# Performance work log

Hardware: AMD Instinct MI355X
Metric: run time of the kernel (lower is better)

Reference implementation:

```python
import jax, jax.numpy as jnp
import numpy as np

NINP = 256
NHID = 256
NOUT = 256
T = 128
B = 256
DIV = 10        # ceil(dt.max()/limit) with dt=1.0, limit=0.1
YCOEFF = 1.0
ZCOEFF = 1.0


def setup_inputs() -> dict:
    key = jax.random.key(0)
    ks = jax.random.split(key, 16)
    std = 1.0 / np.sqrt(NHID)
    u = lambda k, shape: jax.random.uniform(k, shape, jnp.float32, -std, std)
    inp = {
        'input': jax.random.normal(ks[0], (T, B, NINP), jnp.float32),
        'dt': jnp.ones((T, B, 1), jnp.float32),
        'W_i': u(ks[1], (4 * NHID, NINP)),  'b_i': u(ks[2], (4 * NHID,)),
        'W_h': u(ks[3], (3 * NHID, NHID)),  'b_h': u(ks[4], (3 * NHID,)),
        'W_z': u(ks[5], (NHID, NHID)),      'b_z': u(ks[6], (NHID,)),
        'W_dt': u(ks[7], (2, 1)),           'b_dt': u(ks[8], (2,)),
        'W_c': jax.random.normal(ks[9], (NOUT, NHID), jnp.float32) * np.sqrt(2.0 / NHID),
        'b_c': u(ks[10], (NOUT,)),
        'W_s': u(ks[11], (2 * NHID, 2 * NHID)), 'b_s': u(ks[12], (2 * NHID,)),
    }
    return inp


def _forward(input, dt, W_i, b_i, W_h, b_h, W_z, b_z, W_dt, b_dt, W_c, b_c, W_s, b_s):
    noise_key = jax.random.key(1234)
    H = NHID

    def outer(carry, xs):
        y, z = carry
        inp_t, dt_t, t = xs
        delta = dt_t / DIV  # [B, 1]

        def inner(c, d):
            x, y, z = c
            ti = x @ W_i.T + b_i                       # [B, 4H]
            i_dt1, i_dt2, i_z, i_y = jnp.split(ti, 4, axis=1)
            th = y @ W_h.T + b_h                       # [B, 3H]
            h_dt1, h_dt2, h_y = jnp.split(th, 3, axis=1)
            tdt = delta @ W_dt.T + b_dt                # [B, 2]
            t_dt1, t_dt2 = tdt[:, 0:1], tdt[:, 1:2]
            ms_dt_bar = jax.nn.sigmoid(t_dt1) * jax.nn.sigmoid(i_dt1 + h_dt1)
            ms_dt = jax.nn.sigmoid(t_dt2) * jax.nn.sigmoid(i_dt2 + h_dt2)
            z = (1.0 - ms_dt) * z + ms_dt * jnp.tanh(i_y + h_y)
            y = (1.0 - ms_dt_bar) * y + ms_dt_bar * jnp.tanh(z @ W_z.T + b_z + i_z)
            x = y @ W_c.T + b_c                        # classifier output fed back
            k = jax.random.fold_in(noise_key, t * DIV + d)
            noise = jax.random.normal(k, (B, 2 * H), jnp.float32)
            s = jnp.tanh(noise @ W_s.T + b_s)
            ny, nz = s[:, :H], s[:, H:]
            y = y + YCOEFF * ny * delta
            z = z + ZCOEFF * nz * delta
            return (x, y, z), None

        (x, y, z), _ = jax.lax.scan(inner, (inp_t, y, z), jnp.arange(DIV))
        return (y, z), y

    y0 = jnp.zeros((B, H), jnp.float32)
    z0 = jnp.zeros((B, H), jnp.float32)
    (_, _), y_hidds = jax.lax.scan(outer, (y0, z0), (input, dt, jnp.arange(T)))
    out = y_hidds @ W_c.T + b_c  # [T, B, NOUT]
    return out


def reference(input, dt, W_i, b_i, W_h, b_h, W_z, b_z, W_dt, b_dt, W_c, b_c, W_s, b_s):
    return _forward(input, dt, W_i, b_i, W_h, b_h, W_z, b_z, W_dt, b_dt, W_c, b_c, W_s, b_s)
```

## Files before the change

### kernel.cpp

```cpp
#include <hip/hip_runtime.h>
#include <stdint.h>


typedef __attribute__((ext_vector_type(8))) short bf16x8_t;
typedef __attribute__((ext_vector_type(4))) float f32x4_t;
typedef __attribute__((ext_vector_type(4))) unsigned int u32x4_t;
typedef unsigned short u16;

#define R_LDS_BYTES 155904

__device__ __forceinline__ float bf2f(u16 b) {
  union { uint32_t u; float f; } v; v.u = ((uint32_t)b) << 16; return v.f;
}
__device__ __forceinline__ u16 f2bf(float f) {
  union { float f; uint32_t u; } v; v.f = f;
  uint32_t x = v.u;
  return (u16)((x + 0x7FFFu + ((x >> 16) & 1u)) >> 16);
}
__device__ __forceinline__ f32x4_t mfma16(bf16x8_t a, bf16x8_t b, f32x4_t c) {
  return __builtin_amdgcn_mfma_f32_16x16x32_bf16(a, b, c, 0, 0, 0);
}
__device__ __forceinline__ float sigm(float x) { return 1.0f / (1.0f + __expf(-x)); }
__device__ __forceinline__ float tanh_f(float x) {
  float t = __expf(-2.0f * fabsf(x));
  float r = (1.0f - t) / (1.0f + t);
  return x < 0.0f ? -r : r;
}

__device__ __forceinline__ void cstore16(void* p, u32x4_t v) {
  asm volatile("global_store_dwordx4 %0, %1, off sc0 sc1" :: "v"(p), "v"(v) : "memory");
}
__device__ __forceinline__ void pollpair(const uint32_t* p, uint32_t seq,
                                         u32x4_t* a, u32x4_t* b) {
  while (true) {
    u32x4_t x, y;
    asm volatile("global_load_dwordx4 %0, %2, off sc0 sc1\n\t"
                 "global_load_dwordx4 %1, %3, off sc0 sc1\n\t"
                 "s_waitcnt vmcnt(0)"
                 : "=&v"(x), "=&v"(y) : "v"(p), "v"(p + 4) : "memory");
    if (x.y == seq && x.w == seq && y.y == seq && y.w == seq) { *a = x; *b = y; return; }
    __builtin_amdgcn_s_sleep(1);
  }
}
__device__ __forceinline__ u32x4_t cload16v(const void* p) {
  u32x4_t r;
  asm volatile("global_load_dwordx4 %0, %1, off sc0 sc1\n\ts_waitcnt vmcnt(0)"
               : "=&v"(r) : "v"(p) : "memory");
  return r;
}

__device__ __forceinline__ int fragK(int l, int e) {
  return ((l >> 4) << 2) + (e & 3) + ((e >> 2) << 4);
}
__device__ __forceinline__ int halfSlot(int h, int m) {
  return ((h >> 5) & 3) * 512 + (((((h & 15) >> 2) << 4) | m) << 3) +
         ((h & 3) | (((h >> 4) & 1) << 2));
}

__device__ __forceinline__ void threefry(uint32_t k0, uint32_t k1, uint32_t x0, uint32_t x1,
                                         uint32_t* o0, uint32_t* o1) {
  uint32_t ks2 = k0 ^ k1 ^ 0x1BD11BDAu;
  x0 += k0; x1 += k1;
#define TFR(rot) { x0 += x1; x1 = (x1 << rot) | (x1 >> (32 - rot)); x1 ^= x0; }
  TFR(13) TFR(15) TFR(26) TFR(6)   x0 += k1;  x1 += ks2 + 1u;
  TFR(17) TFR(29) TFR(16) TFR(24)  x0 += ks2; x1 += k0 + 2u;
  TFR(13) TFR(15) TFR(26) TFR(6)   x0 += k0;  x1 += k1 + 3u;
  TFR(17) TFR(29) TFR(16) TFR(24)  x0 += k1;  x1 += ks2 + 4u;
  TFR(13) TFR(15) TFR(26) TFR(6)   x0 += ks2; x1 += k0 + 5u;
#undef TFR
  *o0 = x0; *o1 = x1;
}

__device__ __forceinline__ float bits2normal(uint32_t bits) {
  union { uint32_t u; float f; } cv; cv.u = 0x3F800000u | (bits >> 9);
  float f = cv.f - 1.0f;
  float u = fmaf(f, 2.0f, -0.99999994f);
  u = fmaxf(u, -0.99999994f);
  float w = -log1pf(-u * u);
  float p;
  if (w < 5.0f) {
    w = w - 2.5f;
    p = 2.81022636e-08f;
    p = fmaf(p, w, 3.43273939e-07f);
    p = fmaf(p, w, -3.5233877e-06f);
    p = fmaf(p, w, -4.39150654e-06f);
    p = fmaf(p, w, 0.00021858087f);
    p = fmaf(p, w, -0.00125372503f);
    p = fmaf(p, w, -0.00417768164f);
    p = fmaf(p, w, 0.246640727f);
    p = fmaf(p, w, 1.50140941f);
  } else {
    w = sqrtf(w) - 3.0f;
    p = -0.000200214257f;
    p = fmaf(p, w, 0.000100950558f);
    p = fmaf(p, w, 0.00134934322f);
    p = fmaf(p, w, -0.00367342844f);
    p = fmaf(p, w, 0.00573950773f);
    p = fmaf(p, w, -0.0076224613f);
    p = fmaf(p, w, 0.00943887047f);
    p = fmaf(p, w, 1.00167406f);
    p = fmaf(p, w, 2.83297682f);
  }
  return 1.41421354f * p * u;
}

__global__ void k_prep(const float* __restrict__ W_i, const float* __restrict__ W_c,
                       const float* __restrict__ b_i, const float* __restrict__ b_c,
                       float* __restrict__ Wic, float* __restrict__ bip) {
  __shared__ float wi[256];
  __shared__ float red[256];
  int o = blockIdx.x; int tid = threadIdx.x;
  wi[tid] = W_i[o * 256 + tid];
  __syncthreads();
  float acc = 0.f;
  for (int j = 0; j < 256; ++j) acc = fmaf(wi[j], W_c[j * 256 + tid], acc);
  Wic[(size_t)o * 256 + tid] = acc;
  red[tid] = wi[tid] * b_c[tid];
  __syncthreads();
  for (int s = 128; s > 0; s >>= 1) { if (tid < s) red[tid] += red[tid + s]; __syncthreads(); }
  if (tid == 0) bip[o] = b_i[o] + red[0];
}

__global__ void k_bias(const float* __restrict__ b_i, const float* __restrict__ bip,
                       const float* __restrict__ b_h,
                       float* __restrict__ biasD0, float* __restrict__ biasDn) {
  int c = blockIdx.x * 256 + threadIdx.x;
  float bh = (c < 512) ? b_h[c] : (c >= 768 ? b_h[c - 256] : 0.f);
  biasD0[c] = b_i[c] + bh;
  biasDn[c] = bip[c] + bh;
}

__global__ void k_packw(const float* __restrict__ srcA, int rowsA, const float* __restrict__ srcB,
                        u16* __restrict__ dst, int O, int K) {
  int t = blockIdx.x * blockDim.x + threadIdx.x;
  int KK = K >> 5;
  int total = (O >> 4) * KK * 64;
  if (t >= total) return;
  int l = t & 63; int kk = (t >> 6) % KK; int to = t / (64 * KK);
  int n = (to << 4) | (l & 15);
  int kb = (kk << 5) + ((l >> 4) << 2);
  const float* src = (n < rowsA) ? (srcA + (size_t)n * K) : (srcB + (size_t)(n - rowsA) * K);
  u16 out[8];
#pragma unroll
  for (int e = 0; e < 8; ++e) out[e] = f2bf(src[kb + (e & 3) + ((e >> 2) << 4)]);
  *reinterpret_cast<uint4*>(dst + (size_t)t * 8) = *reinterpret_cast<const uint4*>(out);
}

__global__ void k_packe2(const float* __restrict__ Wic, const float* __restrict__ Wh,
                         u16* __restrict__ dst) {
  int t = blockIdx.x * blockDim.x + threadIdx.x;
  int l = t & 63; int kk = (t >> 6) & 7; int to = t >> 9;
  int n = (to << 4) | (l & 15);
  int kb = (kk << 5) + ((l >> 4) << 2);
  u16 out[8];
#pragma unroll
  for (int e = 0; e < 8; ++e) {
    int k = kb + (e & 3) + ((e >> 2) << 4);
    float v = Wic[(size_t)n * 256 + k];
    if (n < 512) v += Wh[(size_t)n * 256 + k];
    else if (n >= 768) v += Wh[(size_t)(n - 256) * 256 + k];
    out[e] = f2bf(v);
  }
  *reinterpret_cast<uint4*>(dst + (size_t)t * 8) = *reinterpret_cast<const uint4*>(out);
}

__global__ void k_packa(const float* __restrict__ inp, int t0, int Tcc, u16* __restrict__ dst) {
  int t = blockIdx.x * blockDim.x + threadIdx.x;
  int total = Tcc * 16 * 8 * 64;
  if (t >= total) return;
  int l = t & 63; int kk = (t >> 6) & 7; int mt = (t >> 9) & 15; int tl = t >> 13;
  int b = (mt << 4) | (l & 15);
  int kb = (kk << 5) + ((l >> 4) << 2);
  const float* src = inp + ((size_t)(t0 + tl) * 256 + b) * 256;
  u16 out[8];
#pragma unroll
  for (int e = 0; e < 8; ++e) out[e] = f2bf(src[kb + (e & 3) + ((e >> 2) << 4)]);
  *reinterpret_cast<uint4*>(dst + (size_t)t * 8) = *reinterpret_cast<const uint4*>(out);
}

__global__ void k_gen(u16* __restrict__ Apack, int gstep0) {
  int sl = blockIdx.x >> 7;
  int tb = (blockIdx.x & 127) * 1024 + threadIdx.x;
  __shared__ uint32_t kf[2];
  if (threadIdx.x == 0) {
    uint32_t o0, o1;
    threefry(0u, 1234u, 0u, (uint32_t)(gstep0 + sl), &o0, &o1);
    kf[0] = o0; kf[1] = o1;
  }
  __syncthreads();
  int e = tb & 7; int l = (tb >> 3) & 63; int kk = (tb >> 9) & 15; int mt = tb >> 13;
  int b = (mt << 4) | (l & 15);
  int c = (kk << 5) + fragK(l, e);
  uint32_t i = (uint32_t)(b * 512 + c);
  uint32_t o0, o1;
  threefry(kf[0], kf[1], 0u, i, &o0, &o1);
  Apack[(size_t)sl * 131072 + tb] = f2bf(bits2normal(o0 ^ o1));
}

__global__ __launch_bounds__(512) void k_sgemm(const u16* __restrict__ Apack,
                                               const u16* __restrict__ Wspack,
                                               const float* __restrict__ b_s,
                                               u16* __restrict__ Sny, u16* __restrict__ Snz,
                                               u16* __restrict__ nyA) {
  int sl = blockIdx.x; int nq = blockIdx.y;
  int l = threadIdx.x & 63; int wv = threadIdx.x >> 6;
  const u16* Ab = Apack + (size_t)sl * 131072;
#pragma unroll 1
  for (int mtl = 0; mtl < 2; ++mtl) {
    int mt = 2 * wv + mtl;
    bf16x8_t af[16];
#pragma unroll
    for (int kk = 0; kk < 16; ++kk)
      af[kk] = *reinterpret_cast<const bf16x8_t*>(Ab + ((size_t)(mt * 16 + kk) * 64 + l) * 8);
#pragma unroll 1
    for (int ntl = 0; ntl < 8; ++ntl) {
      int nt = nq * 8 + ntl;
      f32x4_t acc = {0.f, 0.f, 0.f, 0.f};
#pragma unroll
      for (int kk = 0; kk < 16; ++kk) {
        bf16x8_t bfr = *reinterpret_cast<const bf16x8_t*>(Wspack + ((size_t)(nt * 16 + kk) * 64 + l) * 8);
        acc = mfma16(af[kk], bfr, acc);
      }
      int n = (nt << 4) | (l & 15);
      float bs = b_s[n];
#pragma unroll
      for (int r = 0; r < 4; ++r) {
        int m = (mt << 4) + ((l >> 4) << 2) + r;
        u16 v = f2bf(tanh_f(acc[r] + bs));
        int g = m >> 4, row = m & 15;
        if (n >= 256) {
          int h = n - 256; int hz = h >> 7;
          int tidc = ((h >> 4) & 7) * 64 + ((row >> 2) << 4) + (h & 15);
          Snz[((((size_t)sl * 16 + g) * 2 + hz) * 512 + tidc) * 4 + (row & 3)] = v;
        } else {
          int hy = n >> 7;
          int tidc = ((n >> 4) & 7) * 64 + ((row >> 2) << 4) + (n & 15);
          Sny[((((size_t)sl * 16 + g) * 2 + hy) * 512 + tidc) * 4 + (row & 3)] = v;
          int kk2 = n >> 5;
          int la = (((n & 15) >> 2) << 4) | row;
          int ea = (n & 3) | (((n >> 4) & 1) << 2);
          nyA[(((size_t)sl * 16 + g) * 8 + kk2) * 512 + la * 8 + ea] = v;
        }
      }
    }
  }
}

__global__ __launch_bounds__(512) void k_hn(const u16* __restrict__ nyA,
                                            const u16* __restrict__ Epack,
                                            u16* __restrict__ HNpack, int t0) {
  int j = blockIdx.x; int nq = blockIdx.y;
  int l = threadIdx.x & 63; int wv = threadIdx.x >> 6;
  int nt = nq * 8 + wv;
  if (j == 0 && t0 == 0) {
    uint2 z = {0u, 0u};
#pragma unroll 1
    for (int mt = 0; mt < 16; ++mt)
      *reinterpret_cast<uint2*>(&HNpack[(((size_t)j * 16 + mt) * 48 + nt) * 256 + l * 4]) = z;
    return;
  }
  bf16x8_t bf[8];
  const u16* bp = Epack + (size_t)(64 + nt) * 4096 + (size_t)l * 8;
#pragma unroll
  for (int kk = 0; kk < 8; ++kk)
    bf[kk] = *reinterpret_cast<const bf16x8_t*>(bp + kk * 512);
#pragma unroll 1
  for (int mt = 0; mt < 16; ++mt) {
    const u16* ap = nyA + (((size_t)j * 16 + mt) * 8) * 512 + (size_t)l * 8;
    f32x4_t acc = {0.f, 0.f, 0.f, 0.f};
#pragma unroll
    for (int kk = 0; kk < 8; ++kk)
      acc = mfma16(*reinterpret_cast<const bf16x8_t*>(ap + kk * 512), bf[kk], acc);
    union { u16 h[4]; uint2 v; } o;
#pragma unroll
    for (int r = 0; r < 4; ++r) o.h[r] = f2bf(acc[r]);
    *reinterpret_cast<uint2*>(&HNpack[(((size_t)j * 16 + mt) * 48 + nt) * 256 + l * 4]) = o.v;
  }
}

__global__ __launch_bounds__(512, 2) void k_recur(
    const float* __restrict__ dt,
    const u16* __restrict__ Epack, const u16* __restrict__ Wipack, const u16* __restrict__ Wzpack,
    const u16* __restrict__ E2pack, const u16* __restrict__ HNpack,
    const float* __restrict__ biasD0, const float* __restrict__ biasDn,
    const float* __restrict__ b_z, const float* __restrict__ W_dt, const float* __restrict__ b_dt,
    const u16* __restrict__ inpPack, const u16* __restrict__ Sny, const u16* __restrict__ Snz,
    u16* __restrict__ Ypack, float* __restrict__ ystate, float* __restrict__ ypstate,
    float* __restrict__ zstate,
    uint32_t* __restrict__ yexch, uint32_t* __restrict__ zexch,
    int t0, int Tcc)
{
  extern __shared__ char lds_raw[];
  u16* wlds  = (u16*)lds_raw;
  u16* ypb   = wlds + 65536;
  u16* buf2  = ypb + 4096;
  u16* stage = buf2 + 4096;
  float* sc  = (float*)(stage + 4096);
  float* scP = sc + 48;

  const int wgid = blockIdx.x;
  const int g = wgid & 15;
  const int role = wgid >> 4;
  const bool isY = role < 2;
  const int half = role & 1;
  const int tid = threadIdx.x;
  const int l = tid & 63;
  const int wv = tid >> 6;
  const int nsteps = Tcc * 10;
  const int m2b = 4 * (l >> 4);
  const int col = half * 128 + wv * 16 + (l & 15);
  const uint32_t gb = (uint32_t)(t0 * 10);

  int wiT0, whT0, hnT0, wiT1, whT1 = -1, hnT1 = -1;
  if (isY) {
    wiT0 = half * 8 + wv;       whT0 = 64 + wiT0;  hnT0 = wiT0;
    wiT1 = 32 + half * 8 + wv;
  } else {
    wiT0 = 16 + half * 8 + wv;  whT0 = 64 + wiT0;  hnT0 = wiT0;
    wiT1 = 48 + half * 8 + wv;  whT1 = 96 + half * 8 + wv;  hnT1 = 32 + half * 8 + wv;
  }
  float b0d0 = biasD0[wiT0 * 16 + (l & 15)], b0dn = biasDn[wiT0 * 16 + (l & 15)];
  float b1d0 = biasD0[wiT1 * 16 + (l & 15)], b1dn = biasDn[wiT1 * 16 + (l & 15)];

  for (int i = tid; i < 8192; i += 512) {
    int t = i >> 9; int o = (i & 511) << 3;
    int gt;
    if (isY) gt = (t < 8) ? (half * 8 + t) : (32 + half * 8 + (t - 8));
    else     gt = (t < 8) ? (16 + half * 8 + t) : (48 + half * 8 + (t - 8));
    *reinterpret_cast<uint4*>(wlds + t * 4096 + o) =
        *reinterpret_cast<const uint4*>(E2pack + (size_t)gt * 4096 + o);
  }

  float zc[4], yc[4], ylast[4];
  bf16x8_t wzf[8];
  float bzr = 0.f;

  if (isY) {
    bzr = b_z[col];
#pragma unroll
    for (int kk = 0; kk < 8; ++kk)
      wzf[kk] = *reinterpret_cast<const bf16x8_t*>(
          Wzpack + (size_t)(half * 8 + wv) * 4096 + (size_t)kk * 512 + (size_t)l * 8);
#pragma unroll
    for (int r = 0; r < 4; ++r) {
      int m2 = m2b + r;
      yc[r] = (t0 == 0) ? 0.f : ystate[(size_t)(g * 16 + m2) * 256 + col];
      ylast[r] = 0.f;
      float v = (t0 == 0) ? 0.f : ypstate[(size_t)(g * 16 + m2) * 256 + col];
      stage[halfSlot(col, m2)] = f2bf(v);
    }
    __syncthreads();
    {
      uint2 dv = *reinterpret_cast<const uint2*>(&stage[tid * 4]);
      uint32_t sq = gb + 1u;
      u32x4_t pay = {dv.x, sq, dv.y, sq};
      cstore16(yexch + ((size_t)g * 1024 + half * 512 + tid) * 4, pay);
    }
  } else {
#pragma unroll
    for (int r = 0; r < 4; ++r)
      zc[r] = (t0 == 0) ? 0.f : zstate[(size_t)(g * 16 + m2b + r) * 256 + col];
  }

  float wdt0 = W_dt[0], wdt1 = W_dt[1], bdt0 = b_dt[0], bdt1 = b_dt[1];

  for (int s = 0; s < nsteps; ++s) {
    int d = s % 10, tl = s / 10;
    const u16* SnX = isY ? Sny : Snz;
    uint2 nsv = *reinterpret_cast<const uint2*>(
        SnX + ((((size_t)(s + 1) * 16 + g) * 2 + half) * 512 + tid) * 4);
    size_t HNs = ((size_t)s * 16 + g) * 48;
    uint2 hv0 = *reinterpret_cast<const uint2*>(HNpack + (HNs + hnT0) * 256 + l * 4);
    uint2 hv1 = {0u, 0u};
    if (!isY) hv1 = *reinterpret_cast<const uint2*>(HNpack + (HNs + hnT1) * 256 + l * 4);
    if (d == 0 && tid < 16) {
      float dl = dt[(size_t)(t0 + tl) * 256 + g * 16 + tid] * 0.1f;
      sc[tid] = dl;
      sc[16 + tid] = sigm(fmaf(dl, wdt0, bdt0));
      sc[32 + tid] = sigm(fmaf(dl, wdt1, bdt1));
      int tp = t0 + tl - 1; if (tp < 0) tp = 0;
      scP[tid] = dt[(size_t)tp * 256 + g * 16 + tid] * 0.1f;
    }
    {
      u32x4_t p0, p1;
      pollpair(yexch + (((size_t)(s & 1) * 16 + g) * 1024 + 2 * tid) * 4, gb + (uint32_t)s + 1u,
               &p0, &p1);
      uint2 w0 = {p0.x, p0.z}, w1 = {p1.x, p1.z};
      *reinterpret_cast<uint2*>(ypb + tid * 8) = w0;
      *reinterpret_cast<uint2*>(ypb + tid * 8 + 4) = w1;
      if (d == 0) {
        u16* xb = isY ? stage : buf2;
        *reinterpret_cast<uint4*>(xb + tid * 8) =
            *reinterpret_cast<const uint4*>(inpPack + (size_t)(tl * 16 + g) * 4096 + tid * 8);
      }
    }
    __syncthreads();

    f32x4_t r0, r1;
    {
      bf16x8_t ay[8];
#pragma unroll
      for (int kk = 0; kk < 8; ++kk)
        ay[kk] = *reinterpret_cast<const bf16x8_t*>(ypb + kk * 512 + l * 8);
      float scv[4];
#pragma unroll
      for (int r = 0; r < 4; ++r) scv[r] = (d == 0 ? scP[m2b + r] : sc[m2b + r]);
      f32x4_t a0 = {0.f, 0.f, 0.f, 0.f}, a1 = {0.f, 0.f, 0.f, 0.f};
      if (d == 0) {
        bf16x8_t ax[8];
        const u16* xb = isY ? stage : buf2;
#pragma unroll
        for (int kk = 0; kk < 8; ++kk)
          ax[kk] = *reinterpret_cast<const bf16x8_t*>(xb + kk * 512 + l * 8);
        const u16* bp0 = Wipack + (size_t)wiT0 * 4096 + (size_t)l * 8;
        const u16* hp0 = Epack + (size_t)whT0 * 4096 + (size_t)l * 8;
#pragma unroll
        for (int kk = 0; kk < 8; ++kk)
          a0 = mfma16(ax[kk], *reinterpret_cast<const bf16x8_t*>(bp0 + kk * 512), a0);
#pragma unroll
        for (int kk = 0; kk < 8; ++kk)
          a0 = mfma16(ay[kk], *reinterpret_cast<const bf16x8_t*>(hp0 + kk * 512), a0);
        const u16* bp1 = Wipack + (size_t)wiT1 * 4096 + (size_t)l * 8;
#pragma unroll
        for (int kk = 0; kk < 8; ++kk)
          a1 = mfma16(ax[kk], *reinterpret_cast<const bf16x8_t*>(bp1 + kk * 512), a1);
        if (!isY) {
          const u16* hp1 = Epack + (size_t)whT1 * 4096 + (size_t)l * 8;
#pragma unroll
          for (int kk = 0; kk < 8; ++kk)
            a1 = mfma16(ay[kk], *reinterpret_cast<const bf16x8_t*>(hp1 + kk * 512), a1);
        }
      } else {
        const u16* w0 = wlds + wv * 4096 + l * 8;
        const u16* w1 = wlds + (8 + wv) * 4096 + l * 8;
#pragma unroll
        for (int kk = 0; kk < 8; ++kk)
          a0 = mfma16(ay[kk], *reinterpret_cast<const bf16x8_t*>(w0 + kk * 512), a0);
#pragma unroll
        for (int kk = 0; kk < 8; ++kk)
          a1 = mfma16(ay[kk], *reinterpret_cast<const bf16x8_t*>(w1 + kk * 512), a1);
      }
      const u16* h0 = (const u16*)&hv0;
#pragma unroll
      for (int r = 0; r < 4; ++r)
        r0[r] = a0[r] + (d == 0 ? b0d0 : b0dn) + scv[r] * bf2f(h0[r]);
      if (!isY) {
        const u16* h1 = (const u16*)&hv1;
#pragma unroll
        for (int r = 0; r < 4; ++r)
          r1[r] = a1[r] + (d == 0 ? b1d0 : b1dn) + scv[r] * bf2f(h1[r]);
      } else {
#pragma unroll
        for (int r = 0; r < 4; ++r)
          r1[r] = a1[r] + (d == 0 ? b1d0 : b1dn);
      }
    }

    if (!isY) {
      const u16* nzp = (const u16*)&nsv;
#pragma unroll
      for (int r = 0; r < 4; ++r) {
        int m2 = m2b + r;
        float ms = sc[32 + m2] * sigm(r0[r]);
        float zn = (1.0f - ms) * zc[r] + ms * tanh_f(r1[r]);
        stage[halfSlot(col, m2)] = f2bf(zn);
        zc[r] = fmaf(bf2f(nzp[r]), sc[m2], zn);
      }
      __syncthreads();
      {
        uint2 dv = *reinterpret_cast<const uint2*>(&stage[tid * 4]);
        uint32_t sq = gb + (uint32_t)s + 1u;
        u32x4_t pay = {dv.x, sq, dv.y, sq};
        cstore16(zexch + (((size_t)(s & 1) * 16 + g) * 1024 + half * 512 + tid) * 4, pay);
      }
    } else {
      {
        u32x4_t p0, p1;
        pollpair(zexch + (((size_t)(s & 1) * 16 + g) * 1024 + 2 * tid) * 4, gb + (uint32_t)s + 1u,
                 &p0, &p1);
        uint2 w0 = {p0.x, p0.z}, w1 = {p1.x, p1.z};
        *reinterpret_cast<uint2*>(buf2 + tid * 8) = w0;
        *reinterpret_cast<uint2*>(buf2 + tid * 8 + 4) = w1;
      }
      __syncthreads();
      bf16x8_t zfr[8];
#pragma unroll
      for (int kk = 0; kk < 8; ++kk)
        zfr[kk] = *reinterpret_cast<const bf16x8_t*>(buf2 + kk * 512 + l * 8);
      f32x4_t acc = {0.f, 0.f, 0.f, 0.f};
#pragma unroll
      for (int kk = 0; kk < 8; ++kk) acc = mfma16(zfr[kk], wzf[kk], acc);
      const u16* nyp = (const u16*)&nsv;
      bool last = (d == 9);
#pragma unroll
      for (int r = 0; r < 4; ++r) {
        int m2 = m2b + r;
        float u = acc[r] + bzr + r1[r];
        float msb = sc[16 + m2] * sigm(r0[r]);
        float yn = (1.0f - msb) * yc[r] + msb * tanh_f(u);
        float ypn = fmaf(bf2f(nyp[r]), sc[m2], yn);
        yc[r] = ypn; ylast[r] = yn;
        int slot = halfSlot(col, m2);
        stage[slot] = f2bf(yn);
        if (last) stage[2048 + slot] = f2bf(ypn);
      }
      __syncthreads();
      {
        uint2 dv = *reinterpret_cast<const uint2*>(&stage[tid * 4]);
        uint32_t sq = gb + (uint32_t)s + 2u;
        u32x4_t pay = {dv.x, sq, dv.y, sq};
        cstore16(yexch + (((size_t)((s + 1) & 1) * 16 + g) * 1024 + half * 512 + tid) * 4, pay);
        if (last)
          *reinterpret_cast<uint2*>(Ypack + (size_t)(tl * 16 + g) * 4096 + half * 2048 + tid * 4) =
              *reinterpret_cast<const uint2*>(&stage[2048 + tid * 4]);
      }
    }
  }

  if (isY) {
#pragma unroll
    for (int r = 0; r < 4; ++r) {
      int m2 = m2b + r;
      ystate[(size_t)(g * 16 + m2) * 256 + col] = yc[r];
      ypstate[(size_t)(g * 16 + m2) * 256 + col] = ylast[r];
    }
  } else {
#pragma unroll
    for (int r = 0; r < 4; ++r)
      zstate[(size_t)(g * 16 + m2b + r) * 256 + col] = zc[r];
  }
}

__global__ __launch_bounds__(512) void k_out(const u16* __restrict__ Ypack, const u16* __restrict__ Wcpack,
                                             const float* __restrict__ b_c, float* __restrict__ out, int t0) {
  int tl = blockIdx.x; int mh = blockIdx.y;
  int l = threadIdx.x & 63; int wv = threadIdx.x >> 6;
  int mt = mh * 8 + wv;
  const u16* Ab = Ypack + (size_t)(tl * 16 + mt) * 4096 + (size_t)l * 8;
  bf16x8_t af[8];
#pragma unroll
  for (int kk = 0; kk < 8; ++kk) af[kk] = *reinterpret_cast<const bf16x8_t*>(Ab + kk * 512);
#pragma unroll 1
  for (int nt = 0; nt < 16; ++nt) {
    f32x4_t acc = {0.f, 0.f, 0.f, 0.f};
    const u16* bp = Wcpack + ((size_t)nt * 8 * 64 + l) * 8;
#pragma unroll
    for (int kk = 0; kk < 8; ++kk) {
      bf16x8_t bfr = *reinterpret_cast<const bf16x8_t*>(bp + kk * 512);
      acc = mfma16(af[kk], bfr, acc);
    }
    int n = (nt << 4) | (l & 15);
    float bc = b_c[n];
#pragma unroll
    for (int r = 0; r < 4; ++r) {
      int m = (mt << 4) + ((l >> 4) << 2) + r;
      out[((size_t)(t0 + tl) * 256 + m) * 256 + n] = acc[r] + bc;
    }
  }
}

extern "C" void kernel_launch(void* const* d_in, const int* in_sizes, int n_in,
                              void* d_out, int out_size, void* d_ws, size_t ws_size,
                              hipStream_t stream) {
  const float* input = (const float*)d_in[0];
  const float* dt    = (const float*)d_in[1];
  const float* W_i   = (const float*)d_in[2];
  const float* b_i   = (const float*)d_in[3];
  const float* W_h   = (const float*)d_in[4];
  const float* b_h   = (const float*)d_in[5];
  const float* W_z   = (const float*)d_in[6];
  const float* b_z   = (const float*)d_in[7];
  const float* W_dt  = (const float*)d_in[8];
  const float* b_dt  = (const float*)d_in[9];
  const float* W_c   = (const float*)d_in[10];
  const float* b_c   = (const float*)d_in[11];
  const float* W_s   = (const float*)d_in[12];
  const float* b_s   = (const float*)d_in[13];
  float* out = (float*)d_out;

  char* ws = (char*)d_ws;
  size_t off = 0;
  auto alloc = [&](size_t bytes) -> char* {
    char* p = ws + off; off = (off + bytes + 255) & ~(size_t)255; return p;
  };
  u16* Epack   = (u16*)alloc((size_t)112 * 4096 * 2);
  u16* Wipack  = (u16*)alloc((size_t)64 * 4096 * 2);
  u16* Wzpack  = (u16*)alloc((size_t)16 * 4096 * 2);
  u16* Wcpack  = (u16*)alloc((size_t)16 * 4096 * 2);
  u16* Wspack  = (u16*)alloc((size_t)32 * 16 * 512 * 2);
  u16* E2pack  = (u16*)alloc((size_t)64 * 4096 * 2);
  float* bip   = (float*)alloc(1024 * 4);
  float* biasD0= (float*)alloc(1024 * 4);
  float* biasDn= (float*)alloc(1024 * 4);
  float* Wic   = (float*)alloc((size_t)1024 * 256 * 4);
  float* ystate= (float*)alloc((size_t)256 * 256 * 4);
  float* ypstate=(float*)alloc((size_t)256 * 256 * 4);
  float* zstate= (float*)alloc((size_t)256 * 256 * 4);
  uint32_t* yexch = (uint32_t*)alloc((size_t)2 * 16 * 1024 * 16);
  uint32_t* zexch = (uint32_t*)alloc((size_t)2 * 16 * 1024 * 16);
  size_t fixed = off;
  size_t per_slot = (size_t)131072 * 2 + 65536 * 2 + 65536 * 2 + 65536 * 2;
  size_t per_t = 10 * per_slot + (size_t)10 * 196608 * 2 + 131072 + 131072;
  int Tc = 1;
  if (ws_size > fixed + per_t + per_slot) {
    size_t n = (ws_size - fixed - per_slot) / per_t;
    Tc = (n > 128) ? 128 : (int)n;
  }
  if (Tc < 1) Tc = 1;
  int maxslots = Tc * 10 + 1;
  u16* Apack   = (u16*)alloc((size_t)maxslots * 131072 * 2);
  u16* Sny     = (u16*)alloc((size_t)maxslots * 65536 * 2);
  u16* Snz     = (u16*)alloc((size_t)maxslots * 65536 * 2);
  u16* nyA     = (u16*)alloc((size_t)maxslots * 65536 * 2);
  u16* HNpack  = (u16*)alloc((size_t)(Tc * 10) * 196608 * 2);
  u16* inpPack = (u16*)alloc((size_t)Tc * 16 * 8 * 512 * 2);
  u16* Ypack   = (u16*)alloc((size_t)Tc * 16 * 8 * 512 * 2);

  (void)hipFuncSetAttribute((const void*)k_recur, hipFuncAttributeMaxDynamicSharedMemorySize,
                            R_LDS_BYTES);

  k_prep<<<1024, 256, 0, stream>>>(W_i, W_c, b_i, b_c, Wic, bip);
  k_bias<<<4, 256, 0, stream>>>(b_i, bip, b_h, biasD0, biasDn);
  k_packw<<<(112 * 8 * 64) / 256, 256, 0, stream>>>(Wic, 1024, W_h, Epack, 1792, 256);
  k_packw<<<(64 * 8 * 64) / 256, 256, 0, stream>>>(W_i, 1024, (const float*)nullptr, Wipack, 1024, 256);
  k_packw<<<(16 * 8 * 64) / 256, 256, 0, stream>>>(W_z, 256, (const float*)nullptr, Wzpack, 256, 256);
  k_packw<<<(16 * 8 * 64) / 256, 256, 0, stream>>>(W_c, 256, (const float*)nullptr, Wcpack, 256, 256);
  k_packw<<<(32 * 16 * 64) / 256, 256, 0, stream>>>(W_s, 512, (const float*)nullptr, Wspack, 512, 512);
  k_packe2<<<128, 256, 0, stream>>>(Wic, W_h, E2pack);

  for (int t0 = 0; t0 < 128; t0 += Tc) {
    int Tcc = (128 - t0 < Tc) ? (128 - t0) : Tc;
    int nsteps = Tcc * 10;
    int slots = nsteps + 1;
    k_gen<<<slots * 128, 1024, 0, stream>>>(Apack, t0 * 10 - 1);
    dim3 g2(slots, 4);
    k_sgemm<<<g2, 512, 0, stream>>>(Apack, Wspack, b_s, Sny, Snz, nyA);
    dim3 g3(nsteps, 6);
    k_hn<<<g3, 512, 0, stream>>>(nyA, Epack, HNpack, t0);
    int totalA = Tcc * 16 * 8 * 64;
    k_packa<<<(totalA + 255) / 256, 256, 0, stream>>>(input, t0, Tcc, inpPack);
    k_recur<<<64, 512, R_LDS_BYTES, stream>>>(dt, Epack, Wipack, Wzpack, E2pack, HNpack,
                                              biasD0, biasDn, b_z, W_dt, b_dt, inpPack, Sny, Snz,
                                              Ypack, ystate, ypstate, zstate, yexch, zexch,
                                              t0, Tcc);
    dim3 ge(Tcc, 2);
    k_out<<<ge, 512, 0, stream>>>(Ypack, Wcpack, b_c, out, t0);
  }
}
```

Before: 7.235 ms.

## Hoist input projection out of recurrence and streamline cross-workgroup exchange

Adds a k_xi kernel that precomputes the x@W_i projection for each outer step ahead of time, so the recurrent kernel no longer runs those MFMAs on the critical path. The exchange protocol now writes each payload twice, once with sc0 sc1 and once with sc0 only. Pollers check the sc0 copy first, aiming for lower-latency visibility, and each thread scatters its words into fragment layout itself instead of staging through LDS with extra barriers. The Y workgroups poll only the other half's y, since they already hold their own, and k_out is reworked to read through LDS with more blocks. The cost is extra global writes and workspace, plus some risk around memory-coherence semantics.

```diff
diff --git a/kernel.cpp b/kernel.cpp
--- a/kernel.cpp
+++ b/kernel.cpp
@@ -7,7 +7,7 @@
 typedef __attribute__((ext_vector_type(4))) unsigned int u32x4_t;
 typedef unsigned short u16;
 
-#define R_LDS_BYTES 155904
+#define R_LDS_BYTES 147712
 
 __device__ __forceinline__ float bf2f(u16 b) {
   union { uint32_t u; float f; } v; v.u = ((uint32_t)b) << 16; return v.f;
@@ -27,34 +27,60 @@
   return x < 0.0f ? -r : r;
 }
 
-__device__ __forceinline__ void cstore16(void* p, u32x4_t v) {
-  asm volatile("global_store_dwordx4 %0, %1, off sc0 sc1" :: "v"(p), "v"(v) : "memory");
-}
-__device__ __forceinline__ void pollpair(const uint32_t* p, uint32_t seq,
-                                         u32x4_t* a, u32x4_t* b) {
+__device__ __forceinline__ int fslot(int k, int m) {
+  return ((k >> 5) * 512) + (((((k & 15) >> 2) << 4) | m) << 3) +
+         ((k & 3) | (((k >> 4) & 1) << 2));
+}
+__device__ __forceinline__ int fragK(int l, int e) {
+  return ((l >> 4) << 2) + (e & 3) + ((e >> 2) << 4);
+}
+
+__device__ __forceinline__ void publish(uint32_t* p3, uint32_t* p2,
+                                        uint32_t w0, uint32_t w1, uint32_t seq) {
+  u32x4_t pay; pay.x = w0; pay.y = seq; pay.z = w1; pay.w = seq;
+  asm volatile("global_store_dwordx4 %0, %2, off sc0 sc1\n\t"
+               "global_store_dwordx4 %1, %2, off sc0"
+               :: "v"(p3), "v"(p2), "v"(pay) : "memory");
+}
+__device__ __forceinline__ void pollpair_dual(const uint32_t* p2, const uint32_t* p3,
+                                              uint32_t seq, u32x4_t* a, u32x4_t* b) {
   while (true) {
     u32x4_t x, y;
+    asm volatile("global_load_dwordx4 %0, %2, off sc0\n\t"
+                 "global_load_dwordx4 %1, %3, off sc0\n\t"
+                 "s_waitcnt vmcnt(0)"
+                 : "=&v"(x), "=&v"(y) : "v"(p2), "v"(p2 + 4) : "memory");
+    if (x.y == seq && x.w == seq && y.y == seq && y.w == seq) { *a = x; *b = y; return; }
     asm volatile("global_load_dwordx4 %0, %2, off sc0 sc1\n\t"
                  "global_load_dwordx4 %1, %3, off sc0 sc1\n\t"
                  "s_waitcnt vmcnt(0)"
-                 : "=&v"(x), "=&v"(y) : "v"(p), "v"(p + 4) : "memory");
+                 : "=&v"(x), "=&v"(y) : "v"(p3), "v"(p3 + 4) : "memory");
     if (x.y == seq && x.w == seq && y.y == seq && y.w == seq) { *a = x; *b = y; return; }
     __builtin_amdgcn_s_sleep(1);
   }
 }
-__device__ __forceinline__ u32x4_t cload16v(const void* p) {
-  u32x4_t r;
-  asm volatile("global_load_dwordx4 %0, %1, off sc0 sc1\n\ts_waitcnt vmcnt(0)"
-               : "=&v"(r) : "v"(p) : "memory");
-  return r;
-}
-
-__device__ __forceinline__ int fragK(int l, int e) {
-  return ((l >> 4) << 2) + (e & 3) + ((e >> 2) << 4);
-}
-__device__ __forceinline__ int halfSlot(int h, int m) {
-  return ((h >> 5) & 3) * 512 + (((((h & 15) >> 2) << 4) | m) << 3) +
-         ((h & 3) | (((h >> 4) & 1) << 2));
+__device__ __forceinline__ void poll1_dual(const uint32_t* p2, const uint32_t* p3,
+                                           uint32_t seq, u32x4_t* a) {
+  while (true) {
+    u32x4_t x;
+    asm volatile("global_load_dwordx4 %0, %1, off sc0\n\ts_waitcnt vmcnt(0)"
+                 : "=&v"(x) : "v"(p2) : "memory");
+    if (x.y == seq && x.w == seq) { *a = x; return; }
+    asm volatile("global_load_dwordx4 %0, %1, off sc0 sc1\n\ts_waitcnt vmcnt(0)"
+                 : "=&v"(x) : "v"(p3) : "memory");
+    if (x.y == seq && x.w == seq) { *a = x; return; }
+    __builtin_amdgcn_s_sleep(1);
+  }
+}
+__device__ __forceinline__ void scatter2(u16* dst, int j, u32x4_t p) {
+  int wvp = (j >> 6) & 7, lp = j & 63, hf = j >> 9;
+  int colp = hf * 128 + wvp * 16 + (lp & 15);
+  int mb = 4 * (lp >> 4);
+  int base = fslot(colp, mb);
+  dst[base]      = (u16)(p.x & 0xffffu);
+  dst[base + 8]  = (u16)(p.x >> 16);
+  dst[base + 16] = (u16)(p.z & 0xffffu);
+  dst[base + 24] = (u16)(p.z >> 16);
 }
 
 __device__ __forceinline__ void threefry(uint32_t k0, uint32_t k1, uint32_t x0, uint32_t x1,
@@ -278,24 +304,49 @@
   }
 }
 
+__global__ __launch_bounds__(512) void k_xi(const u16* __restrict__ inpPack,
+                                            const u16* __restrict__ Wipack,
+                                            u16* __restrict__ XIpack) {
+  int tl = blockIdx.x; int nb = blockIdx.y;
+  int l = threadIdx.x & 63; int wv = threadIdx.x >> 6;
+  int nt = nb * 8 + wv;
+  bf16x8_t bf[8];
+  const u16* bp = Wipack + (size_t)nt * 4096 + (size_t)l * 8;
+#pragma unroll
+  for (int kk = 0; kk < 8; ++kk)
+    bf[kk] = *reinterpret_cast<const bf16x8_t*>(bp + kk * 512);
+#pragma unroll 1
+  for (int g = 0; g < 16; ++g) {
+    const u16* ap = inpPack + (size_t)(tl * 16 + g) * 4096 + (size_t)l * 8;
+    f32x4_t acc = {0.f, 0.f, 0.f, 0.f};
+#pragma unroll
+    for (int kk = 0; kk < 8; ++kk)
+      acc = mfma16(*reinterpret_cast<const bf16x8_t*>(ap + kk * 512), bf[kk], acc);
+    union { u16 h[4]; uint2 v; } o;
+#pragma unroll
+    for (int r = 0; r < 4; ++r) o.h[r] = f2bf(acc[r]);
+    *reinterpret_cast<uint2*>(&XIpack[(((size_t)tl * 16 + g) * 64 + nt) * 256 + l * 4]) = o.v;
+  }
+}
+
 __global__ __launch_bounds__(512, 2) void k_recur(
     const float* __restrict__ dt,
-    const u16* __restrict__ Epack, const u16* __restrict__ Wipack, const u16* __restrict__ Wzpack,
+    const u16* __restrict__ Epack, const u16* __restrict__ Wzpack,
     const u16* __restrict__ E2pack, const u16* __restrict__ HNpack,
+    const u16* __restrict__ XIpack,
     const float* __restrict__ biasD0, const float* __restrict__ biasDn,
     const float* __restrict__ b_z, const float* __restrict__ W_dt, const float* __restrict__ b_dt,
-    const u16* __restrict__ inpPack, const u16* __restrict__ Sny, const u16* __restrict__ Snz,
+    const u16* __restrict__ Sny, const u16* __restrict__ Snz,
     u16* __restrict__ Ypack, float* __restrict__ ystate, float* __restrict__ ypstate,
     float* __restrict__ zstate,
-    uint32_t* __restrict__ yexch, uint32_t* __restrict__ zexch,
+    uint32_t* __restrict__ yexch, uint32_t* __restrict__ yexch2,
+    uint32_t* __restrict__ zexch, uint32_t* __restrict__ zexch2,
     int t0, int Tcc)
 {
   extern __shared__ char lds_raw[];
-  u16* wlds  = (u16*)lds_raw;
-  u16* ypb   = wlds + 65536;
-  u16* buf2  = ypb + 4096;
-  u16* stage = buf2 + 4096;
-  float* sc  = (float*)(stage + 4096);
+  u16* wlds = (u16*)lds_raw;
+  u16* buf  = wlds + 65536;
+  float* sc  = (float*)(buf + 8192);
   float* scP = sc + 48;
 
   const int wgid = blockIdx.x;
@@ -334,6 +385,7 @@
   float zc[4], yc[4], ylast[4];
   bf16x8_t wzf[8];
   float bzr = 0.f;
+  float wdt0 = W_dt[0], wdt1 = W_dt[1], bdt0 = b_dt[0], bdt1 = b_dt[1];
 
   if (isY) {
     bzr = b_z[col];
@@ -341,207 +393,247 @@
     for (int kk = 0; kk < 8; ++kk)
       wzf[kk] = *reinterpret_cast<const bf16x8_t*>(
           Wzpack + (size_t)(half * 8 + wv) * 4096 + (size_t)kk * 512 + (size_t)l * 8);
+    u16 v[4];
 #pragma unroll
     for (int r = 0; r < 4; ++r) {
       int m2 = m2b + r;
       yc[r] = (t0 == 0) ? 0.f : ystate[(size_t)(g * 16 + m2) * 256 + col];
       ylast[r] = 0.f;
-      float v = (t0 == 0) ? 0.f : ypstate[(size_t)(g * 16 + m2) * 256 + col];
-      stage[halfSlot(col, m2)] = f2bf(v);
+      float vv = (t0 == 0) ? 0.f : ypstate[(size_t)(g * 16 + m2) * 256 + col];
+      v[r] = f2bf(vv);
     }
-    __syncthreads();
-    {
-      uint2 dv = *reinterpret_cast<const uint2*>(&stage[tid * 4]);
-      uint32_t sq = gb + 1u;
-      u32x4_t pay = {dv.x, sq, dv.y, sq};
-      cstore16(yexch + ((size_t)g * 1024 + half * 512 + tid) * 4, pay);
-    }
+    int base = fslot(col, m2b);
+    buf[base] = v[0]; buf[base + 8] = v[1]; buf[base + 16] = v[2]; buf[base + 24] = v[3];
+    uint32_t w0 = (uint32_t)v[0] | ((uint32_t)v[1] << 16);
+    uint32_t w1 = (uint32_t)v[2] | ((uint32_t)v[3] << 16);
+    size_t so = ((size_t)g * 1024 + half * 512 + tid) * 4;
+    publish(yexch + so, yexch2 + so, w0, w1, gb + 1u);
   } else {
 #pragma unroll
     for (int r = 0; r < 4; ++r)
       zc[r] = (t0 == 0) ? 0.f : zstate[(size_t)(g * 16 + m2b + r) * 256 + col];
   }
 
-  float wdt0 = W_dt[0], wdt1 = W_dt[1], bdt0 = b_dt[0], bdt1 = b_dt[1];
-
-  for (int s = 0; s < nsteps; ++s) {
-    int d = s % 10, tl = s / 10;
-    const u16* SnX = isY ? Sny : Snz;
-    uint2 nsv = *reinterpret_cast<const uint2*>(
-        SnX + ((((size_t)(s + 1) * 16 + g) * 2 + half) * 512 + tid) * 4);
-    size_t HNs = ((size_t)s * 16 + g) * 48;
-    uint2 hv0 = *reinterpret_cast<const uint2*>(HNpack + (HNs + hnT0) * 256 + l * 4);
-    uint2 hv1 = {0u, 0u};
-    if (!isY) hv1 = *reinterpret_cast<const uint2*>(HNpack + (HNs + hnT1) * 256 + l * 4);
-    if (d == 0 && tid < 16) {
-      float dl = dt[(size_t)(t0 + tl) * 256 + g * 16 + tid] * 0.1f;
-      sc[tid] = dl;
-      sc[16 + tid] = sigm(fmaf(dl, wdt0, bdt0));
-      sc[32 + tid] = sigm(fmaf(dl, wdt1, bdt1));
-      int tp = t0 + tl - 1; if (tp < 0) tp = 0;
-      scP[tid] = dt[(size_t)tp * 256 + g * 16 + tid] * 0.1f;
-    }
-    {
-      u32x4_t p0, p1;
-      pollpair(yexch + (((size_t)(s & 1) * 16 + g) * 1024 + 2 * tid) * 4, gb + (uint32_t)s + 1u,
-               &p0, &p1);
-      uint2 w0 = {p0.x, p0.z}, w1 = {p1.x, p1.z};
-      *reinterpret_cast<uint2*>(ypb + tid * 8) = w0;
-      *reinterpret_cast<uint2*>(ypb + tid * 8 + 4) = w1;
+  if (!isY) {
+    for (int s = 0; s < nsteps; ++s) {
+      int d = s % 10;
+      uint2 nsv = *reinterpret_cast<const uint2*>(
+          Snz + ((((size_t)(s + 1) * 16 + g) * 2 + half) * 512 + tid) * 4);
+      size_t HNs = ((size_t)s * 16 + g) * 48;
+      uint2 hv0 = *reinterpret_cast<const uint2*>(HNpack + (HNs + hnT0) * 256 + l * 4);
+      uint2 hv1 = *reinterpret_cast<const uint2*>(HNpack + (HNs + hnT1) * 256 + l * 4);
+      uint2 xi0 = {0u, 0u}, xi1 = {0u, 0u};
       if (d == 0) {
-        u16* xb = isY ? stage : buf2;
-        *reinterpret_cast<uint4*>(xb + tid * 8) =
-            *reinterpret_cast<const uint4*>(inpPack + (size_t)(tl * 16 + g) * 4096 + tid * 8);
-      }
-    }
-    __syncthreads();
-
-    f32x4_t r0, r1;
-    {
+        int tl = s / 10;
+        size_t XIs = ((size_t)tl * 16 + g) * 64;
+        xi0 = *reinterpret_cast<const uint2*>(XIpack + (XIs + wiT0) * 256 + l * 4);
+        xi1 = *reinterpret_cast<const uint2*>(XIpack + (XIs + wiT1) * 256 + l * 4);
+        if (tid < 16) {
+          float dl = dt[(size_t)(t0 + tl) * 256 + g * 16 + tid] * 0.1f;
+          sc[tid] = dl;
+          sc[16 + tid] = sigm(fmaf(dl, wdt0, bdt0));
+          sc[32 + tid] = sigm(fmaf(dl, wdt1, bdt1));
+          int tp = t0 + tl - 1; if (tp < 0) tp = 0;
+          scP[tid] = dt[(size_t)tp * 256 + g * 16 + tid] * 0.1f;
+        }
+      }
+      uint32_t seq = gb + (uint32_t)s + 1u;
+      size_t bo = (((size_t)(s & 1) * 16 + g) * 1024 + 2 * tid) * 4;
+      u32x4_t pa, pb;
+      pollpair_dual(yexch2 + bo, yexch + bo, seq, &pa, &pb);
+      u16* yb = buf + (s & 1) * 4096;
+      scatter2(yb, 2 * tid, pa);
+      scatter2(yb, 2 * tid + 1, pb);
+      __syncthreads();
       bf16x8_t ay[8];
 #pragma unroll
       for (int kk = 0; kk < 8; ++kk)
-        ay[kk] = *reinterpret_cast<const bf16x8_t*>(ypb + kk * 512 + l * 8);
+        ay[kk] = *reinterpret_cast<const bf16x8_t*>(yb + kk * 512 + l * 8);
       float scv[4];
 #pragma unroll
       for (int r = 0; r < 4; ++r) scv[r] = (d == 0 ? scP[m2b + r] : sc[m2b + r]);
       f32x4_t a0 = {0.f, 0.f, 0.f, 0.f}, a1 = {0.f, 0.f, 0.f, 0.f};
       if (d == 0) {
-        bf16x8_t ax[8];
-        const u16* xb = isY ? stage : buf2;
-#pragma unroll
-        for (int kk = 0; kk < 8; ++kk)
-          ax[kk] = *reinterpret_cast<const bf16x8_t*>(xb + kk * 512 + l * 8);
-        const u16* bp0 = Wipack + (size_t)wiT0 * 4096 + (size_t)l * 8;
         const u16* hp0 = Epack + (size_t)whT0 * 4096 + (size_t)l * 8;
-#pragma unroll
-        for (int kk = 0; kk < 8; ++kk)
-          a0 = mfma16(ax[kk], *reinterpret_cast<const bf16x8_t*>(bp0 + kk * 512), a0);
+        const u16* hp1 = Epack + (size_t)whT1 * 4096 + (size_t)l * 8;
 #pragma unroll
         for (int kk = 0; kk < 8; ++kk)
           a0 = mfma16(ay[kk], *reinterpret_cast<const bf16x8_t*>(hp0 + kk * 512), a0);
-        const u16* bp1 = Wipack + (size_t)wiT1 * 4096 + (size_t)l * 8;
 #pragma unroll
         for (int kk = 0; kk < 8; ++kk)
-          a1 = mfma16(ax[kk], *reinterpret_cast<const bf16x8_t*>(bp1 + kk * 512), a1);
-        if (!isY) {
-          const u16* hp1 = Epack + (size_t)whT1 * 4096 + (size_t)l * 8;
-#pragma unroll
-          for (int kk = 0; kk < 8; ++kk)
-            a1 = mfma16(ay[kk], *reinterpret_cast<const bf16x8_t*>(hp1 + kk * 512), a1);
-        }
+          a1 = mfma16(ay[kk], *reinterpret_cast<const bf16x8_t*>(hp1 + kk * 512), a1);
       } else {
-        const u16* w0 = wlds + wv * 4096 + l * 8;
-        const u16* w1 = wlds + (8 + wv) * 4096 + l * 8;
+        const u16* w0p = wlds + wv * 4096 + l * 8;
+        const u16* w1p = wlds + (8 + wv) * 4096 + l * 8;
 #pragma unroll
         for (int kk = 0; kk < 8; ++kk)
-          a0 = mfma16(ay[kk], *reinterpret_cast<const bf16x8_t*>(w0 + kk * 512), a0);
+          a0 = mfma16(ay[kk], *reinterpret_cast<const bf16x8_t*>(w0p + kk * 512), a0);
 #pragma unroll
         for (int kk = 0; kk < 8; ++kk)
-          a1 = mfma16(ay[kk], *reinterpret_cast<const bf16x8_t*>(w1 + kk * 512), a1);
-      }
-      const u16* h0 = (const u16*)&hv0;
-#pragma unroll
-      for (int r = 0; r < 4; ++r)
-        r0[r] = a0[r] + (d == 0 ? b0d0 : b0dn) + scv[r] * bf2f(h0[r]);
-      if (!isY) {
-        const u16* h1 = (const u16*)&hv1;
-#pragma unroll
-        for (int r = 0; r < 4; ++r)
-          r1[r] = a1[r] + (d == 0 ? b1d0 : b1dn) + scv[r] * bf2f(h1[r]);
-      } else {
-#pragma unroll
-        for (int r = 0; r < 4; ++r)
-          r1[r] = a1[r] + (d == 0 ? b1d0 : b1dn);
-      }
-    }
-
-    if (!isY) {
+          a1 = mfma16(ay[kk], *reinterpret_cast<const bf16x8_t*>(w1p + kk * 512), a1);
+      }
+      const u16* h0 = (const u16*)&hv0; const u16* h1 = (const u16*)&hv1;
+      const u16* x0 = (const u16*)&xi0; const u16* x1 = (const u16*)&xi1;
       const u16* nzp = (const u16*)&nsv;
+      u16 zv[4];
 #pragma unroll
       for (int r = 0; r < 4; ++r) {
         int m2 = m2b + r;
-        float ms = sc[32 + m2] * sigm(r0[r]);
-        float zn = (1.0f - ms) * zc[r] + ms * tanh_f(r1[r]);
-        stage[halfSlot(col, m2)] = f2bf(zn);
+        float r0 = a0[r] + (d == 0 ? (b0d0 + bf2f(x0[r])) : b0dn) + scv[r] * bf2f(h0[r]);
+        float r1 = a1[r] + (d == 0 ? (b1d0 + bf2f(x1[r])) : b1dn) + scv[r] * bf2f(h1[r]);
+        float ms = sc[32 + m2] * sigm(r0);
+        float zn = (1.0f - ms) * zc[r] + ms * tanh_f(r1);
+        zv[r] = f2bf(zn);
         zc[r] = fmaf(bf2f(nzp[r]), sc[m2], zn);
       }
+      uint32_t w0z = (uint32_t)zv[0] | ((uint32_t)zv[1] << 16);
+      uint32_t w1z = (uint32_t)zv[2] | ((uint32_t)zv[3] << 16);
+      size_t so = (((size_t)(s & 1) * 16 + g) * 1024 + half * 512 + tid) * 4;
+      publish(zexch + so, zexch2 + so, w0z, w1z, seq);
+    }
+#pragma unroll
+    for (int r = 0; r < 4; ++r)
+      zstate[(size_t)(g * 16 + m2b + r) * 256 + col] = zc[r];
+  } else {
+    for (int s = 0; s < nsteps; ++s) {
+      int d = s % 10, tl = s / 10;
+      uint2 nsv = *reinterpret_cast<const uint2*>(
+          Sny + ((((size_t)(s + 1) * 16 + g) * 2 + half) * 512 + tid) * 4);
+      size_t HNs = ((size_t)s * 16 + g) * 48;
+      uint2 hv0 = *reinterpret_cast<const uint2*>(HNpack + (HNs + hnT0) * 256 + l * 4);
+      uint2 xi0 = {0u, 0u}, xi1 = {0u, 0u};
+      if (d == 0) {
+        size_t XIs = ((size_t)tl * 16 + g) * 64;
+        xi0 = *reinterpret_cast<const uint2*>(XIpack + (XIs + wiT0) * 256 + l * 4);
+        xi1 = *reinterpret_cast<const uint2*>(XIpack + (XIs + wiT1) * 256 + l * 4);
+        if (tid < 16) {
+          float dl = dt[(size_t)(t0 + tl) * 256 + g * 16 + tid] * 0.1f;
+          sc[tid] = dl;
+          sc[16 + tid] = sigm(fmaf(dl, wdt0, bdt0));
+          sc[32 + tid] = sigm(fmaf(dl, wdt1, bdt1));
+          int tp = t0 + tl - 1; if (tp < 0) tp = 0;
+          scP[tid] = dt[(size_t)tp * 256 + g * 16 + tid] * 0.1f;
+        }
+      }
+      uint32_t seq = gb + (uint32_t)s + 1u;
+      {
+        int j = ((1 ^ half) * 512 + tid);
+        size_t bo = (((size_t)(s & 1) * 16 + g) * 1024 + j) * 4;
+        u32x4_t pa;
+        poll1_dual(yexch2 + bo, yexch + bo, seq, &pa);
+        scatter2(buf, j, pa);
+      }
       __syncthreads();
+      f32x4_t r0v, r1v;
       {
-        uint2 dv = *reinterpret_cast<const uint2*>(&stage[tid * 4]);
-        uint32_t sq = gb + (uint32_t)s + 1u;
-        u32x4_t pay = {dv.x, sq, dv.y, sq};
-        cstore16(zexch + (((size_t)(s & 1) * 16 + g) * 1024 + half * 512 + tid) * 4, pay);
-      }
-    } else {
+        bf16x8_t ay[8];
+#pragma unroll
+        for (int kk = 0; kk < 8; ++kk)
+          ay[kk] = *reinterpret_cast<const bf16x8_t*>(buf + kk * 512 + l * 8);
+        float scv[4];
+#pragma unroll
+        for (int r = 0; r < 4; ++r) scv[r] = (d == 0 ? scP[m2b + r] : sc[m2b + r]);
+        f32x4_t a0 = {0.f, 0.f, 0.f, 0.f}, a1 = {0.f, 0.f, 0.f, 0.f};
+        if (d == 0) {
+          const u16* hp0 = Epack + (size_t)whT0 * 4096 + (size_t)l * 8;
+#pragma unroll
+          for (int kk = 0; kk < 8; ++kk)
+            a0 = mfma16(ay[kk], *reinterpret_cast<const bf16x8_t*>(hp0 + kk * 512), a0);
+        } else {
+          const u16* w0p = wlds + wv * 4096 + l * 8;
+          const u16* w1p = wlds + (8 + wv) * 4096 + l * 8;
+#pragma unroll
+          for (int kk = 0; kk < 8; ++kk)
+            a0 = mfma16(ay[kk], *reinterpret_cast<const bf16x8_t*>(w0p + kk * 512), a0);
+#pragma unroll
+          for (int kk = 0; kk < 8; ++kk)
+            a1 = mfma16(ay[kk], *reinterpret_cast<const bf16x8_t*>(w1p + kk * 512), a1);
+        }
+        const u16* h0 = (const u16*)&hv0;
+        const u16* x0 = (const u16*)&xi0; const u16* x1 = (const u16*)&xi1;
+#pragma unroll
+        for (int r = 0; r < 4; ++r) {
+          r0v[r] = a0[r] + (d == 0 ? (b0d0 + bf2f(x0[r])) : b0dn) + scv[r] * bf2f(h0[r]);
+          r1v[r] = (d == 0) ? (b1d0 + bf2f(x1[r])) : (a1[r] + b1dn);
+        }
+      }
       {
-        u32x4_t p0, p1;
-        pollpair(zexch + (((size_t)(s & 1) * 16 + g) * 1024 + 2 * tid) * 4, gb + (uint32_t)s + 1u,
-                 &p0, &p1);
-        uint2 w0 = {p0.x, p0.z}, w1 = {p1.x, p1.z};
-        *reinterpret_cast<uint2*>(buf2 + tid * 8) = w0;
-        *reinterpret_cast<uint2*>(buf2 + tid * 8 + 4) = w1;
+        size_t bo = (((size_t)(s & 1) * 16 + g) * 1024 + 2 * tid) * 4;
+        u32x4_t qa, qb;
+        pollpair_dual(zexch2 + bo, zexch + bo, seq, &qa, &qb);
+        u16* zb = buf + 4096;
+        scatter2(zb, 2 * tid, qa);
+        scatter2(zb, 2 * tid + 1, qb);
       }
       __syncthreads();
       bf16x8_t zfr[8];
 #pragma unroll
       for (int kk = 0; kk < 8; ++kk)
-        zfr[kk] = *reinterpret_cast<const bf16x8_t*>(buf2 + kk * 512 + l * 8);
+        zfr[kk] = *reinterpret_cast<const bf16x8_t*>(buf + 4096 + kk * 512 + l * 8);
       f32x4_t acc = {0.f, 0.f, 0.f, 0.f};
 #pragma unroll
       for (int kk = 0; kk < 8; ++kk) acc = mfma16(zfr[kk], wzf[kk], acc);
       const u16* nyp = (const u16*)&nsv;
-      bool last = (d == 9);
+      u16 yv[4], pv[4];
+      int base = fslot(col, m2b);
 #pragma unroll
       for (int r = 0; r < 4; ++r) {
         int m2 = m2b + r;
-        float u = acc[r] + bzr + r1[r];
-        float msb = sc[16 + m2] * sigm(r0[r]);
+        float u = acc[r] + bzr + r1v[r];
+        float msb = sc[16 + m2] * sigm(r0v[r]);
         float yn = (1.0f - msb) * yc[r] + msb * tanh_f(u);
         float ypn = fmaf(bf2f(nyp[r]), sc[m2], yn);
         yc[r] = ypn; ylast[r] = yn;
-        int slot = halfSlot(col, m2);
-        stage[slot] = f2bf(yn);
-        if (last) stage[2048 + slot] = f2bf(ypn);
-      }
-      __syncthreads();
-      {
-        uint2 dv = *reinterpret_cast<const uint2*>(&stage[tid * 4]);
-        uint32_t sq = gb + (uint32_t)s + 2u;
-        u32x4_t pay = {dv.x, sq, dv.y, sq};
-        cstore16(yexch + (((size_t)((s + 1) & 1) * 16 + g) * 1024 + half * 512 + tid) * 4, pay);
-        if (last)
-          *reinterpret_cast<uint2*>(Ypack + (size_t)(tl * 16 + g) * 4096 + half * 2048 + tid * 4) =
-              *reinterpret_cast<const uint2*>(&stage[2048 + tid * 4]);
+        yv[r] = f2bf(yn); pv[r] = f2bf(ypn);
+        buf[base + 8 * r] = yv[r];
+      }
+      uint32_t wy0 = (uint32_t)yv[0] | ((uint32_t)yv[1] << 16);
+      uint32_t wy1 = (uint32_t)yv[2] | ((uint32_t)yv[3] << 16);
+      size_t so = (((size_t)((s + 1) & 1) * 16 + g) * 1024 + half * 512 + tid) * 4;
+      publish(yexch + so, yexch2 + so, wy0, wy1, gb + (uint32_t)s + 2u);
+      if (d == 9) {
+        uint2 pp = {(uint32_t)pv[0] | ((uint32_t)pv[1] << 16),
+                    (uint32_t)pv[2] | ((uint32_t)pv[3] << 16)};
+        *reinterpret_cast<uint2*>(Ypack + (size_t)(tl * 16 + g) * 4096 + (half * 512 + tid) * 4) = pp;
       }
     }
-  }
-
-  if (isY) {
 #pragma unroll
     for (int r = 0; r < 4; ++r) {
       int m2 = m2b + r;
       ystate[(size_t)(g * 16 + m2) * 256 + col] = yc[r];
       ypstate[(size_t)(g * 16 + m2) * 256 + col] = ylast[r];
     }
-  } else {
-#pragma unroll
-    for (int r = 0; r < 4; ++r)
-      zstate[(size_t)(g * 16 + m2b + r) * 256 + col] = zc[r];
   }
 }
 
 __global__ __launch_bounds__(512) void k_out(const u16* __restrict__ Ypack, const u16* __restrict__ Wcpack,
                                              const float* __restrict__ b_c, float* __restrict__ out, int t0) {
+  __shared__ u16 yl[4 * 4096];
   int tl = blockIdx.x; int mh = blockIdx.y;
-  int l = threadIdx.x & 63; int wv = threadIdx.x >> 6;
-  int mt = mh * 8 + wv;
-  const u16* Ab = Ypack + (size_t)(tl * 16 + mt) * 4096 + (size_t)l * 8;
+  int tid = threadIdx.x; int l = tid & 63; int wv = tid >> 6;
+  for (int i = tid; i < 4096; i += 512) {
+    int pg = i >> 10; int j = i & 1023;
+    uint2 v = *reinterpret_cast<const uint2*>(
+        Ypack + ((size_t)(tl * 16 + mh * 4 + pg)) * 4096 + (size_t)j * 4);
+    int wvp = (j >> 6) & 7, lp = j & 63, hf = j >> 9;
+    int colp = hf * 128 + wvp * 16 + (lp & 15);
+    int mb = 4 * (lp >> 4);
+    int base = pg * 4096 + fslot(colp, mb);
+    yl[base] = (u16)(v.x & 0xffffu);
+    yl[base + 8] = (u16)(v.x >> 16);
+    yl[base + 16] = (u16)(v.y & 0xffffu);
+    yl[base + 24] = (u16)(v.y >> 16);
+  }
+  __syncthreads();
+  int gl = wv >> 1; int nh = wv & 1;
+  int mt = mh * 4 + gl;
   bf16x8_t af[8];
 #pragma unroll
-  for (int kk = 0; kk < 8; ++kk) af[kk] = *reinterpret_cast<const bf16x8_t*>(Ab + kk * 512);
+  for (int kk = 0; kk < 8; ++kk)
+    af[kk] = *reinterpret_cast<const bf16x8_t*>(yl + gl * 4096 + kk * 512 + l * 8);
 #pragma unroll 1
-  for (int nt = 0; nt < 16; ++nt) {
+  for (int ntl = 0; ntl < 8; ++ntl) {
+    int nt = nh * 8 + ntl;
     f32x4_t acc = {0.f, 0.f, 0.f, 0.f};
     const u16* bp = Wcpack + ((size_t)nt * 8 * 64 + l) * 8;
 #pragma unroll
@@ -596,11 +688,13 @@
   float* ystate= (float*)alloc((size_t)256 * 256 * 4);
   float* ypstate=(float*)alloc((size_t)256 * 256 * 4);
   float* zstate= (float*)alloc((size_t)256 * 256 * 4);
-  uint32_t* yexch = (uint32_t*)alloc((size_t)2 * 16 * 1024 * 16);
-  uint32_t* zexch = (uint32_t*)alloc((size_t)2 * 16 * 1024 * 16);
+  uint32_t* yexch  = (uint32_t*)alloc((size_t)2 * 16 * 1024 * 16);
+  uint32_t* yexch2 = (uint32_t*)alloc((size_t)2 * 16 * 1024 * 16);
+  uint32_t* zexch  = (uint32_t*)alloc((size_t)2 * 16 * 1024 * 16);
+  uint32_t* zexch2 = (uint32_t*)alloc((size_t)2 * 16 * 1024 * 16);
   size_t fixed = off;
   size_t per_slot = (size_t)131072 * 2 + 65536 * 2 + 65536 * 2 + 65536 * 2;
-  size_t per_t = 10 * per_slot + (size_t)10 * 196608 * 2 + 131072 + 131072;
+  size_t per_t = 10 * per_slot + (size_t)10 * 196608 * 2 + 131072 + 131072 + 524288;
   int Tc = 1;
   if (ws_size > fixed + per_t + per_slot) {
     size_t n = (ws_size - fixed - per_slot) / per_t;
@@ -614,6 +708,7 @@
   u16* nyA     = (u16*)alloc((size_t)maxslots * 65536 * 2);
   u16* HNpack  = (u16*)alloc((size_t)(Tc * 10) * 196608 * 2);
   u16* inpPack = (u16*)alloc((size_t)Tc * 16 * 8 * 512 * 2);
+  u16* XIpack  = (u16*)alloc((size_t)Tc * 524288);
   u16* Ypack   = (u16*)alloc((size_t)Tc * 16 * 8 * 512 * 2);
 
   (void)hipFuncSetAttribute((const void*)k_recur, hipFuncAttributeMaxDynamicSharedMemorySize,
@@ -639,11 +734,13 @@
     k_hn<<<g3, 512, 0, stream>>>(nyA, Epack, HNpack, t0);
     int totalA = Tcc * 16 * 8 * 64;
     k_packa<<<(totalA + 255) / 256, 256, 0, stream>>>(input, t0, Tcc, inpPack);
-    k_recur<<<64, 512, R_LDS_BYTES, stream>>>(dt, Epack, Wipack, Wzpack, E2pack, HNpack,
-                                              biasD0, biasDn, b_z, W_dt, b_dt, inpPack, Sny, Snz,
-                                              Ypack, ystate, ypstate, zstate, yexch, zexch,
-                                              t0, Tcc);
-    dim3 ge(Tcc, 2);
+    dim3 gx(Tcc, 8);
+    k_xi<<<gx, 512, 0, stream>>>(inpPack, Wipack, XIpack);
+    k_recur<<<64, 512, R_LDS_BYTES, stream>>>(dt, Epack, Wzpack, E2pack, HNpack, XIpack,
+                                              biasD0, biasDn, b_z, W_dt, b_dt, Sny, Snz,
+                                              Ypack, ystate, ypstate, zstate,
+                                              yexch, yexch2, zexch, zexch2, t0, Tcc);
+    dim3 ge(Tcc, 4);
     k_out<<<ge, 512, 0, stream>>>(Ypack, Wcpack, b_c, out, t0);
   }
 }
```

Measured after the change: 7.106 ms. No clear change (-1.8%).
